# Kernel tuning notes

Measured on AMD Instinct MI355X. Metric: run time of the kernel, lower is better.

The kernel has to match this reference:

```python
import jax, jax.numpy as jnp
import numpy as np

K = 4            # kNN neighbors (edge_conv k=4)
HEADS = 4
HID = 32
NEG_SLOPE = 0.2  # PyG GATConv leaky_relu default


def knn_idx(x, k):
    # x: [N, C]. Pairwise squared distances via gram trick, self excluded.
    N = x.shape[0]
    sq = jnp.sum(x * x, axis=1)
    d = sq[:, None] + sq[None, :] - 2.0 * (x @ x.T)          # [N, N]
    r = jnp.arange(N)
    d = d.at[r, r].set(jnp.inf)                               # no self in kNN
    _, idx = jax.lax.top_k(-d, k)                             # [N, k] nearest
    return idx


def gat_layer(x, neigh, W, a_src, a_dst, b):
    # x: [N, C]; neigh: [N, k+1] (incl. self loop). PyG GATConv, concat=True.
    N = x.shape[0]
    h = (x @ W).reshape(N, HEADS, HID)                        # [N, H, D]
    asrc = jnp.einsum('nhd,hd->nh', h, a_src)                 # [N, H]
    adst = jnp.einsum('nhd,hd->nh', h, a_dst)                 # [N, H]
    e = jax.nn.leaky_relu(adst[:, None, :] + asrc[neigh], NEG_SLOPE)  # [N, k+1, H]
    attn = jax.nn.softmax(e, axis=1)                          # segment softmax (fixed fan-in)
    out = jnp.einsum('nkh,nkhd->nhd', attn, h[neigh])         # [N, H, D]
    return out.reshape(N, HEADS * HID) + b


def setup_inputs() -> dict:
    key = jax.random.key(0)
    ks = jax.random.split(key, 12)
    B, E, C = 256, 64, 32
    s = 0.1
    return {
        'x': jax.random.normal(ks[0], (B, E, C), jnp.float32),
        # DynamicEdgeConv MLP: Linear(2C->HID), ReLU, Linear(HID->HID)
        'mlp_w1': jax.random.normal(ks[1], (2 * C, HID), jnp.float32) * s,
        'mlp_b1': jnp.zeros((HID,), jnp.float32),
        'mlp_w2': jax.random.normal(ks[2], (HID, HID), jnp.float32) * s,
        'mlp_b2': jnp.zeros((HID,), jnp.float32),
        # GATConv(HID, HID, heads=HEADS, concat=True)
        'gat_w': jax.random.normal(ks[3], (C, HEADS * HID), jnp.float32) * s,
        'gat_asrc': jax.random.normal(ks[4], (HEADS, HID), jnp.float32) * s,
        'gat_adst': jax.random.normal(ks[5], (HEADS, HID), jnp.float32) * s,
        'gat_b': jnp.zeros((HEADS * HID,), jnp.float32),
        # fc: Linear(HID*HEADS -> num_classes)
        'fc_w': jax.random.normal(ks[6], (HEADS * HID, 2), jnp.float32) * s,
        'fc_b': jnp.zeros((2,), jnp.float32),
    }


def reference(x, mlp_w1, mlp_b1, mlp_w2, mlp_b2, gat_w, gat_asrc, gat_adst, gat_b, fc_w, fc_b):
    B, E, C = x.shape
    N = B * E
    xf = x.reshape(N, C)
    idx = knn_idx(xf, K)                                      # [N, K] int32
    # EdgeConv message MLP + max pool (edge_attr is discarded by the original forward)
    xi = xf[:, None, :]                                       # [N, 1, C]
    xj = xf[idx]                                              # [N, K, C]
    ef = jnp.concatenate([jnp.broadcast_to(xi, xj.shape), xj - xi], axis=-1)
    ef = jax.nn.relu(ef @ mlp_w1 + mlp_b1) @ mlp_w2 + mlp_b2
    _edge_attr = ef.max(axis=1)                               # [N, HID], unused downstream
    # GAT with self loops (PyG add_self_loops=True)
    neigh = jnp.concatenate([idx, jnp.arange(N)[:, None]], axis=1)  # [N, K+1]
    h = gat_layer(xf, neigh, gat_w, gat_asrc, gat_adst, gat_b)
    h = jax.nn.elu(h)
    h = h.reshape(B, E, HEADS * HID).mean(axis=1)             # [B, H*D]
    return h @ fc_w + fc_b                                    # [B, num_classes]
```

## Files before the change

kernel.cpp:

```cpp
#include <hip/hip_runtime.h>
#include <math.h>

#define N_PTS   16384
#define NT      1024
#define NCHUNK  32
#define JT_CH   (NT/NCHUNK)
#define SUBT    16
#define NSUB    (JT_CH/SUBT)
#define NS      16
#define JSPLIT  4
#define NPB     256

typedef __attribute__((ext_vector_type(4))) float f32x4;
typedef __attribute__((ext_vector_type(8))) _Float16 half8;

union H8 { half8 h; float4 f; };

#define MED3(a,b,c) __builtin_amdgcn_fmed3f((a),(b),(c))

#define INS4(c, A0, A1, A2, A3) {        \
  float n0_ = fmaxf(A0, c);              \
  float n1_ = MED3(A0, A1, c);           \
  float n2_ = MED3(A1, A2, c);           \
  float n3_ = MED3(A2, A3, c);           \
  A0 = n0_; A1 = n1_; A2 = n2_; A3 = n3_; }

__device__ __forceinline__ unsigned long long pack_key(float a, int j) {
  unsigned u = __float_as_uint(a);
  unsigned ord = u ^ (unsigned)(((int)u >> 31) | 0x80000000);
  unsigned m = ~ord;
  return ((unsigned long long)m << 32) | (unsigned)j;
}

__global__ __launch_bounds__(64) void k_prep(
    const float* __restrict__ x, float4* __restrict__ fragHi,
    float4* __restrict__ fragLo, float* __restrict__ nsq,
    unsigned* __restrict__ gcnt, unsigned long long* __restrict__ gbuf,
    unsigned* __restrict__ bcnt, float2* __restrict__ pmax)
{
  int p = blockIdx.x * 64 + threadIdx.x;
  const float4* xp = (const float4*)(x + (size_t)p * 32);
  int tile = p >> 4, lb = p & 15;
  float sq = 0.f, hn2 = 0.f, ln2 = 0.f;
  #pragma unroll
  for (int g = 0; g < 4; ++g) {
    float4 va = xp[g * 2], vb = xp[g * 2 + 1];
    float f[8] = {va.x, va.y, va.z, va.w, vb.x, vb.y, vb.z, vb.w};
    H8 hh, hl;
    #pragma unroll
    for (int e = 0; e < 8; ++e) {
      sq = fmaf(f[e], f[e], sq);
      _Float16 hi = (_Float16)f[e];
      _Float16 lo = (_Float16)(f[e] - (float)hi);
      hh.h[e] = hi; hl.h[e] = lo;
      float hf = (float)hi, lf = (float)lo;
      hn2 = fmaf(hf, hf, hn2);
      ln2 = fmaf(lf, lf, ln2);
    }
    int a = tile * 64 + g * 16 + lb;
    fragHi[a] = hh.f; fragLo[a] = hl.f;
  }
  nsq[p] = -0.5f * sq;
  gcnt[p] = 0u;
  #pragma unroll
  for (int e = 0; e < NS; ++e) gbuf[(size_t)p * NS + e] = ~0ull;
  if (blockIdx.x == 0 && threadIdx.x < NCHUNK) bcnt[threadIdx.x] = 0u;

  #pragma unroll
  for (int off = 32; off; off >>= 1) {
    hn2 = fmaxf(hn2, __shfl_xor(hn2, off));
    ln2 = fmaxf(ln2, __shfl_xor(ln2, off));
  }
  if (threadIdx.x == 0) pmax[blockIdx.x] = make_float2(hn2, ln2);
}

__global__ __launch_bounds__(256, 4) void k_knnA(
    const float4* __restrict__ fragHi, const float* __restrict__ nsq,
    float* __restrict__ cvals,
    const float* __restrict__ x, const float* __restrict__ gw,
    const float* __restrict__ aw_s, const float* __restrict__ aw_d,
    float* __restrict__ h, float* __restrict__ asrc, float* __restrict__ adst)
{
  __shared__ half8 sHi[SUBT * 64];
  __shared__ float sNq[SUBT * 16];

  const int tid = threadIdx.x;
  const int cy = blockIdx.y;

  if (cy >= NCHUNK) {
    const int fb = (cy - NCHUNK) * 64 + blockIdx.x;
    const int d = tid & 127, half = tid >> 7;
    const int head = d >> 5, hid = d & 31;

    float gwr[32];
    #pragma unroll
    for (int k = 0; k < 32; ++k) gwr[k] = gw[k * 128 + d];
    const float ws_ = aw_s[head * 32 + hid], wd_ = aw_d[head * 32 + hid];

    #pragma unroll
    for (int p = 0; p < 8; ++p) {
      int nl = (p << 1) | half;
      int n = fb * 16 + nl;
      const float4* xr = (const float4*)(x + (size_t)n * 32);
      float acc = 0.f;
      #pragma unroll
      for (int r = 0; r < 8; ++r) {
        float4 v = xr[r];
        acc = fmaf(v.x, gwr[r * 4 + 0], acc);
        acc = fmaf(v.y, gwr[r * 4 + 1], acc);
        acc = fmaf(v.z, gwr[r * 4 + 2], acc);
        acc = fmaf(v.w, gwr[r * 4 + 3], acc);
      }
      h[(size_t)n * 128 + d] = acc;
      float ps = acc * ws_, pd = acc * wd_;
      #pragma unroll
      for (int off = 16; off; off >>= 1) {
        ps += __shfl_xor(ps, off, 32);
        pd += __shfl_xor(pd, off, 32);
      }
      if (hid == 0) { asrc[n * 4 + head] = ps; adst[n * 4 + head] = pd; }
    }
    return;
  }

  const int w = tid >> 6, lane = tid & 63;
  const int grp = lane >> 4, col = lane & 15;
  const int itbase = blockIdx.x * 16 + w * 4;
  const bool blkdiag = ((int)(blockIdx.x >> 1) == cy);

  const half8* fH8 = (const half8*)fragHi;

  half8 bh[4];
  #pragma unroll
  for (int s = 0; s < 4; ++s)
    bh[s] = fH8[(size_t)(itbase + s) * 64 + lane];
  const bool dg0 = (col == grp * 4 + 0), dg1 = (col == grp * 4 + 1);
  const bool dg2 = (col == grp * 4 + 2), dg3 = (col == grp * 4 + 3);

  float La1[4];
  #pragma unroll
  for (int s = 0; s < 4; ++s) La1[s] = -3.4e38f;

  for (int sc = 0; sc < NSUB; ++sc) {
    int jt0 = cy * JT_CH + sc * SUBT;
    __syncthreads();
    const float4* gH = fragHi + (size_t)jt0 * 64;
    float4* dH = (float4*)sHi;
    #pragma unroll
    for (int r = 0; r < 4; ++r)
      dH[tid + r * 256] = gH[tid + r * 256];
    sNq[tid] = nsq[jt0 * 16 + tid];
    __syncthreads();

    for (int t = 0; t < SUBT; ++t) {
      half8 ah = sHi[t * 64 + lane];
      f32x4 q = *(const f32x4*)&sNq[t * 16 + grp * 4];
      int jt = jt0 + t;
      #pragma unroll
      for (int s = 0; s < 4; ++s) {
        f32x4 acc = __builtin_amdgcn_mfma_f32_16x16x32_f16(ah, bh[s], q, 0, 0, 0);
        if (blkdiag && jt == itbase + s) {
          acc.x = dg0 ? -3.4e38f : acc.x;
          acc.y = dg1 ? -3.4e38f : acc.y;
          acc.z = dg2 ? -3.4e38f : acc.z;
          acc.w = dg3 ? -3.4e38f : acc.w;
        }
        float t3 = fmaxf(fmaxf(acc.x, acc.y), acc.z);
        La1[s] = fmaxf(fmaxf(t3, acc.w), La1[s]);
      }
    }
  }

  #pragma unroll
  for (int s = 0; s < 4; ++s) {
    float m = La1[s];
    m = fmaxf(m, __shfl_xor(m, 16));
    m = fmaxf(m, __shfl_xor(m, 32));
    if (grp == 0) {
      int row = (itbase + s) * 16 + col;
      cvals[(size_t)cy * N_PTS + row] = m;
    }
  }
}

__global__ __launch_bounds__(128) void k_tauwl(
    const float* __restrict__ cvals, float* __restrict__ tau,
    unsigned* __restrict__ bcnt, int* __restrict__ bucket,
    const float2* __restrict__ pmax)
{
  __shared__ unsigned lcnt[NCHUNK];
  __shared__ unsigned gbase[NCHUNK];
  __shared__ int stage[NCHUNK][64];
  __shared__ float4 sL[64];
  __shared__ float sT[64];
  __shared__ float sEps;

  const int tid = threadIdx.x;
  const int lrow = tid & 63, half = tid >> 6;
  const int row = blockIdx.x * 64 + lrow;
  if (tid < NCHUNK) lcnt[tid] = 0u;

  if (tid < 64) {
    float hm = 0.f, lm = 0.f;
    #pragma unroll
    for (int k = 0; k < NPB / 64; ++k) {
      float2 v = pmax[tid + k * 64];
      hm = fmaxf(hm, v.x);
      lm = fmaxf(lm, v.y);
    }
    #pragma unroll
    for (int off = 32; off; off >>= 1) {
      hm = fmaxf(hm, __shfl_xor(hm, off));
      lm = fmaxf(lm, __shfl_xor(lm, off));
    }
    if (tid == 0) sEps = 4.4f * sqrtf(hm) * sqrtf(lm) + 1e-3f;
  }
  __syncthreads();
  const float eps = sEps;

  float A0 = -3.4e38f, A1 = -3.4e38f, A2 = -3.4e38f, A3 = -3.4e38f;
  float cm[16];
  #pragma unroll
  for (int k = 0; k < 16; ++k) {
    cm[k] = cvals[(size_t)(half * 16 + k) * N_PTS + row];
    INS4(cm[k], A0, A1, A2, A3);
  }
  if (half == 1) sL[lrow] = make_float4(A0, A1, A2, A3);
  __syncthreads();
  if (half == 0) {
    float4 o = sL[lrow];
    INS4(o.x, A0, A1, A2, A3);
    INS4(o.y, A0, A1, A2, A3);
    INS4(o.z, A0, A1, A2, A3);
    INS4(o.w, A0, A1, A2, A3);
    float theta = A3 - eps;
    sT[lrow] = theta;
    tau[row] = theta;
  }
  __syncthreads();
  const float tt = sT[lrow];
  #pragma unroll
  for (int k = 0; k < 16; ++k) {
    if (cm[k] >= tt) {
      int c = half * 16 + k;
      unsigned p = atomicAdd(&lcnt[c], 1u);
      stage[c][p] = row;
    }
  }
  __syncthreads();
  if (tid < NCHUNK) gbase[tid] = atomicAdd(bcnt + tid, lcnt[tid]);
  __syncthreads();
  for (int c = 0; c < NCHUNK; ++c) {
    unsigned n = lcnt[c], gb = gbase[c];
    for (unsigned k = tid; k < n; k += 128)
      bucket[c * N_PTS + gb + k] = stage[c][k];
  }
}

__global__ __launch_bounds__(256) void k_knnBW(
    const float4* __restrict__ fragHi, const float4* __restrict__ fragLo,
    const float* __restrict__ nsq, const float* __restrict__ tau,
    const unsigned* __restrict__ bcnt, const int* __restrict__ bucket,
    unsigned* __restrict__ gcnt, unsigned long long* __restrict__ gbuf)
{
  const int c = blockIdx.x;
  const int jseg = blockIdx.y >> 8;
  const unsigned n = bcnt[c];
  const unsigned base = (unsigned)(blockIdx.y & 255) * 64;
  if (base >= n) return;

  __shared__ int   sRow[64];
  __shared__ float sTau[64];

  const int tid = threadIdx.x;
  const int w = tid >> 6, lane = tid & 63;
  const int grp = lane >> 4, col = lane & 15;
  const float INF = __int_as_float(0x7f800000);

  if (tid < 64) {
    unsigned idx = base + tid;
    int myrow = (idx < n) ? bucket[c * N_PTS + idx] : -1;
    sRow[tid] = myrow;
    sTau[tid] = (myrow >= 0) ? tau[myrow] : INF;
  }
  __syncthreads();

  const half8* fH8 = (const half8*)fragHi;
  const half8* fL8 = (const half8*)fragLo;

  half8 bh[4], bl[4];
  int   rS[4];
  float tS[4];
  #pragma unroll
  for (int s = 0; s < 4; ++s) {
    int r = sRow[s * 16 + col];
    rS[s] = r;
    tS[s] = sTau[s * 16 + col];
    int rr = r < 0 ? 0 : r;
    size_t a = (size_t)(rr >> 4) * 64 + grp * 16 + (rr & 15);
    bh[s] = fH8[a];
    bl[s] = fL8[a];
  }

  const int jt0 = c * JT_CH + jseg * (JT_CH / JSPLIT) + w * (JT_CH / (JSPLIT * 4));
  #pragma unroll
  for (int ti = 0; ti < JT_CH / (JSPLIT * 4); ++ti) {
    int jt = jt0 + ti;
    half8 ah = fH8[(size_t)jt * 64 + lane];
    half8 al = fL8[(size_t)jt * 64 + lane];
    f32x4 q = *(const f32x4*)&nsq[jt * 16 + grp * 4];
    #pragma unroll
    for (int s = 0; s < 4; ++s) {
      f32x4 acc = __builtin_amdgcn_mfma_f32_16x16x32_f16(ah, bh[s], q, 0, 0, 0);
      acc = __builtin_amdgcn_mfma_f32_16x16x32_f16(ah, bl[s], acc, 0, 0, 0);
      acc = __builtin_amdgcn_mfma_f32_16x16x32_f16(al, bh[s], acc, 0, 0, 0);
      int jbase = jt * 16 + grp * 4;
      acc.x = (jbase + 0 == rS[s]) ? -3.4e38f : acc.x;
      acc.y = (jbase + 1 == rS[s]) ? -3.4e38f : acc.y;
      acc.z = (jbase + 2 == rS[s]) ? -3.4e38f : acc.z;
      acc.w = (jbase + 3 == rS[s]) ? -3.4e38f : acc.w;
      float m = fmaxf(fmaxf(acc.x, acc.y), fmaxf(acc.z, acc.w));
      if (__ballot(m >= tS[s])) {
        float av[4] = {acc.x, acc.y, acc.z, acc.w};
        #pragma unroll
        for (int e = 0; e < 4; ++e) {
          if (av[e] >= tS[s]) {
            unsigned sl = atomicAdd(gcnt + rS[s], 1u);
            if (sl < (unsigned)NS) gbuf[(size_t)rS[s] * NS + sl] = pack_key(av[e], jbase + e);
          }
        }
      }
    }
  }
}

__global__ __launch_bounds__(256) void k_gat(
    const float* __restrict__ h, const float* __restrict__ asrc, const float* __restrict__ adst,
    const unsigned long long* __restrict__ gbuf, const float* __restrict__ gb,
    float* __restrict__ mo_part)
{
  int b2 = blockIdx.x;
  int b = b2 >> 2, qq = b2 & 3;
  int tid = threadIdx.x;
  __shared__ int4 sknn[16];
  if (tid < 16) {
    int row = b * 64 + qq * 16 + tid;
    unsigned long long K0 = ~0ull, K1 = ~0ull, K2 = ~0ull, K3 = ~0ull;
    const unsigned long long* src = gbuf + (size_t)row * NS;
    #pragma unroll
    for (int e = 0; e < NS; ++e) {
      unsigned long long cc = src[e];
      bool g = cc < K3, c0 = cc < K0, c1 = cc < K1, c2 = cc < K2;
      unsigned long long n1 = c0 ? K0 : (c1 ? cc : K1);
      unsigned long long n2 = c1 ? K1 : (c2 ? cc : K2);
      unsigned long long n3 = c2 ? K2 : (g ? cc : K3);
      K0 = c0 ? cc : K0; K1 = n1; K2 = n2; K3 = n3;
    }
    sknn[tid] = make_int4((int)(unsigned)K0, (int)(unsigned)K1,
                          (int)(unsigned)K2, (int)(unsigned)K3);
  }
  __syncthreads();

  int w = tid >> 6, lane = tid & 63;
  int da = lane, db = lane + 64;
  int ha = lane >> 5, hb = ha + 2;
  float acca = 0.f, accb = 0.f;

  #pragma unroll
  for (int t = 0; t < 4; ++t) {
    int nl = t * 4 + w;
    int n = b * 64 + qq * 16 + nl;
    int4 nb = sknn[nl];
    int nbs[5] = {nb.x, nb.y, nb.z, nb.w, n};
    float ad_a = adst[n * 4 + ha], ad_b = adst[n * 4 + hb];
    float ea[5], eb[5];
    #pragma unroll
    for (int k = 0; k < 5; ++k) {
      float va = ad_a + asrc[nbs[k] * 4 + ha];
      float vb = ad_b + asrc[nbs[k] * 4 + hb];
      ea[k] = va > 0.f ? va : 0.2f * va;
      eb[k] = vb > 0.f ? vb : 0.2f * vb;
    }
    float ma = ea[0], mb = eb[0];
    #pragma unroll
    for (int k = 1; k < 5; ++k) { ma = fmaxf(ma, ea[k]); mb = fmaxf(mb, eb[k]); }
    float sa = 0.f, sb = 0.f;
    #pragma unroll
    for (int k = 0; k < 5; ++k) {
      ea[k] = __expf(ea[k] - ma); sa += ea[k];
      eb[k] = __expf(eb[k] - mb); sb += eb[k];
    }
    float outa = 0.f, outb = 0.f;
    #pragma unroll
    for (int k = 0; k < 5; ++k) {
      const float* hr = h + (size_t)nbs[k] * 128;
      outa = fmaf(ea[k], hr[da], outa);
      outb = fmaf(eb[k], hr[db], outb);
    }
    outa = outa / sa + gb[da];
    outb = outb / sb + gb[db];
    acca += outa > 0.f ? outa : expm1f(outa);
    accb += outb > 0.f ? outb : expm1f(outb);
  }

  __shared__ float red[4][128];
  red[w][da] = acca; red[w][db] = accb;
  __syncthreads();
  if (tid < 128) {
    float s = (red[0][tid] + red[1][tid] + red[2][tid] + red[3][tid]) * (1.f / 64.f);
    mo_part[b2 * 128 + tid] = s;
  }
}

__global__ __launch_bounds__(64) void k_fc(
    const float* __restrict__ mo_part, const float* __restrict__ fw, const float* __restrict__ fb,
    float* __restrict__ out)
{
  int b = blockIdx.x, lane = threadIdx.x;
  float m0 = 0.f, m1 = 0.f;
  #pragma unroll
  for (int q = 0; q < 4; ++q) {
    m0 += mo_part[(b * 4 + q) * 128 + lane];
    m1 += mo_part[(b * 4 + q) * 128 + lane + 64];
  }
  float p0 = m0 * fw[lane * 2]     + m1 * fw[(lane + 64) * 2];
  float p1 = m0 * fw[lane * 2 + 1] + m1 * fw[(lane + 64) * 2 + 1];
  #pragma unroll
  for (int off = 32; off; off >>= 1) {
    p0 += __shfl_xor(p0, off, 64);
    p1 += __shfl_xor(p1, off, 64);
  }
  if (lane == 0) { out[b * 2] = p0 + fb[0]; out[b * 2 + 1] = p1 + fb[1]; }
}

extern "C" void kernel_launch(void* const* d_in, const int* in_sizes, int n_in,
                              void* d_out, int out_size, void* d_ws, size_t ws_size,
                              hipStream_t stream)
{
  const float* x   = (const float*)d_in[0];
  const float* gw  = (const float*)d_in[5];
  const float* as_ = (const float*)d_in[6];
  const float* ad_ = (const float*)d_in[7];
  const float* gb  = (const float*)d_in[8];
  const float* fw  = (const float*)d_in[9];
  const float* fb  = (const float*)d_in[10];

  char* ws = (char*)d_ws;
  float*  cvals  = (float*)(ws);
  float*  h      = (float*)(ws + 2097152);
  float*  asrc   = (float*)(ws + 10485760);
  float*  adst   = (float*)(ws + 10747904);
  float4* fragHi = (float4*)(ws + 11010048);
  float4* fragLo = (float4*)(ws + 12058624);
  float*  nsq    = (float*)(ws + 13107200);
  float*  tau    = (float*)(ws + 13172736);
  unsigned* gcnt = (unsigned*)(ws + 13238272);
  unsigned long long* gbuf = (unsigned long long*)(ws + 13303808);
  unsigned* bcnt = (unsigned*)(ws + 15400960);
  float2* pmax   = (float2*)(ws + 15401216);
  int*    bucket = (int*)   (ws + 15403264);
  float*  mo_part= (float*)(ws + 17500416);
  float*  outp   = (float*)d_out;

  k_prep<<<NPB, 64, 0, stream>>>(x, fragHi, fragLo, nsq, gcnt, gbuf, bcnt, pmax);
  k_knnA<<<dim3(64, NCHUNK + 16), 256, 0, stream>>>(fragHi, nsq, cvals,
                                                    x, gw, as_, ad_, h, asrc, adst);
  k_tauwl<<<N_PTS / 64, 128, 0, stream>>>(cvals, tau, bcnt, bucket, pmax);
  k_knnBW<<<dim3(NCHUNK, 256 * JSPLIT), 256, 0, stream>>>(fragHi, fragLo, nsq, tau,
                                                          bcnt, bucket, gcnt, gbuf);
  k_gat<<<1024, 256, 0, stream>>>(h, asrc, adst, gbuf, gb, mo_part);
  k_fc<<<256, 64, 0, stream>>>(mo_part, fw, fb, outp);
}
```

Baseline: 94.26 us.

## Refine kNN candidate pruning to sub-chunk granularity of 16 tiles

The coarse pass now records a per-row max for each 16-tile sub-chunk (64 sub-chunks instead of 32 chunks). The threshold kernel buckets rows per sub-chunk, and the exact pass launches one block column per sub-chunk over only 16 tiles. Rows are re-checked only against sub-chunks that can contain a near neighbour, which cuts exact-pass work. In exchange it doubles cvals storage and reads, adds work and register pressure to the threshold kernel, and moves the workspace layout around.

Measured after the change: 197.5 us. +109.5%, slower.

```diff
diff --git a/kernel.cpp b/kernel.cpp
--- a/kernel.cpp
+++ b/kernel.cpp
@@ -7,8 +7,9 @@
 #define JT_CH   (NT/NCHUNK)
 #define SUBT    16
 #define NSUB    (JT_CH/SUBT)
+#define NSC     (NCHUNK*NSUB)
+#define JT_SC   16
 #define NS      16
-#define JSPLIT  4
 #define NPB     256
 
 typedef __attribute__((ext_vector_type(4))) float f32x4;
@@ -64,7 +65,7 @@
   gcnt[p] = 0u;
   #pragma unroll
   for (int e = 0; e < NS; ++e) gbuf[(size_t)p * NS + e] = ~0ull;
-  if (blockIdx.x == 0 && threadIdx.x < NCHUNK) bcnt[threadIdx.x] = 0u;
+  if (blockIdx.x == 0 && threadIdx.x < NSC) bcnt[threadIdx.x] = 0u;
 
   #pragma unroll
   for (int off = 32; off; off >>= 1) {
@@ -137,10 +138,6 @@
   const bool dg0 = (col == grp * 4 + 0), dg1 = (col == grp * 4 + 1);
   const bool dg2 = (col == grp * 4 + 2), dg3 = (col == grp * 4 + 3);
 
-  float La1[4];
-  #pragma unroll
-  for (int s = 0; s < 4; ++s) La1[s] = -3.4e38f;
-
   for (int sc = 0; sc < NSUB; ++sc) {
     int jt0 = cy * JT_CH + sc * SUBT;
     __syncthreads();
@@ -151,6 +148,10 @@
       dH[tid + r * 256] = gH[tid + r * 256];
     sNq[tid] = nsq[jt0 * 16 + tid];
     __syncthreads();
+
+    float La1[4];
+    #pragma unroll
+    for (int s = 0; s < 4; ++s) La1[s] = -3.4e38f;
 
     for (int t = 0; t < SUBT; ++t) {
       half8 ah = sHi[t * 64 + lane];
@@ -169,16 +170,16 @@
         La1[s] = fmaxf(fmaxf(t3, acc.w), La1[s]);
       }
     }
-  }
-
-  #pragma unroll
-  for (int s = 0; s < 4; ++s) {
-    float m = La1[s];
-    m = fmaxf(m, __shfl_xor(m, 16));
-    m = fmaxf(m, __shfl_xor(m, 32));
-    if (grp == 0) {
-      int row = (itbase + s) * 16 + col;
-      cvals[(size_t)cy * N_PTS + row] = m;
+
+    #pragma unroll
+    for (int s = 0; s < 4; ++s) {
+      float m = La1[s];
+      m = fmaxf(m, __shfl_xor(m, 16));
+      m = fmaxf(m, __shfl_xor(m, 32));
+      if (grp == 0) {
+        int row = (itbase + s) * 16 + col;
+        cvals[(size_t)(cy * NSUB + sc) * N_PTS + row] = m;
+      }
     }
   }
 }
@@ -188,9 +189,9 @@
     unsigned* __restrict__ bcnt, int* __restrict__ bucket,
     const float2* __restrict__ pmax)
 {
-  __shared__ unsigned lcnt[NCHUNK];
-  __shared__ unsigned gbase[NCHUNK];
-  __shared__ int stage[NCHUNK][64];
+  __shared__ unsigned lcnt[NSC];
+  __shared__ unsigned gbase[NSC];
+  __shared__ int stage[NSC][64];
   __shared__ float4 sL[64];
   __shared__ float sT[64];
   __shared__ float sEps;
@@ -198,7 +199,7 @@
   const int tid = threadIdx.x;
   const int lrow = tid & 63, half = tid >> 6;
   const int row = blockIdx.x * 64 + lrow;
-  if (tid < NCHUNK) lcnt[tid] = 0u;
+  if (tid < NSC) lcnt[tid] = 0u;
 
   if (tid < 64) {
     float hm = 0.f, lm = 0.f;
@@ -219,10 +220,10 @@
   const float eps = sEps;
 
   float A0 = -3.4e38f, A1 = -3.4e38f, A2 = -3.4e38f, A3 = -3.4e38f;
-  float cm[16];
-  #pragma unroll
-  for (int k = 0; k < 16; ++k) {
-    cm[k] = cvals[(size_t)(half * 16 + k) * N_PTS + row];
+  float cm[32];
+  #pragma unroll
+  for (int k = 0; k < 32; ++k) {
+    cm[k] = cvals[(size_t)(half * 32 + k) * N_PTS + row];
     INS4(cm[k], A0, A1, A2, A3);
   }
   if (half == 1) sL[lrow] = make_float4(A0, A1, A2, A3);
@@ -240,17 +241,17 @@
   __syncthreads();
   const float tt = sT[lrow];
   #pragma unroll
-  for (int k = 0; k < 16; ++k) {
+  for (int k = 0; k < 32; ++k) {
     if (cm[k] >= tt) {
-      int c = half * 16 + k;
+      int c = half * 32 + k;
       unsigned p = atomicAdd(&lcnt[c], 1u);
       stage[c][p] = row;
     }
   }
   __syncthreads();
-  if (tid < NCHUNK) gbase[tid] = atomicAdd(bcnt + tid, lcnt[tid]);
-  __syncthreads();
-  for (int c = 0; c < NCHUNK; ++c) {
+  if (tid < NSC) gbase[tid] = atomicAdd(bcnt + tid, lcnt[tid]);
+  __syncthreads();
+  for (int c = 0; c < NSC; ++c) {
     unsigned n = lcnt[c], gb = gbase[c];
     for (unsigned k = tid; k < n; k += 128)
       bucket[c * N_PTS + gb + k] = stage[c][k];
@@ -264,9 +265,8 @@
     unsigned* __restrict__ gcnt, unsigned long long* __restrict__ gbuf)
 {
   const int c = blockIdx.x;
-  const int jseg = blockIdx.y >> 8;
   const unsigned n = bcnt[c];
-  const unsigned base = (unsigned)(blockIdx.y & 255) * 64;
+  const unsigned base = blockIdx.y * 64;
   if (base >= n) return;
 
   __shared__ int   sRow[64];
@@ -302,9 +302,9 @@
     bl[s] = fL8[a];
   }
 
-  const int jt0 = c * JT_CH + jseg * (JT_CH / JSPLIT) + w * (JT_CH / (JSPLIT * 4));
-  #pragma unroll
-  for (int ti = 0; ti < JT_CH / (JSPLIT * 4); ++ti) {
+  const int jt0 = c * JT_SC + w * (JT_SC / 4);
+  #pragma unroll
+  for (int ti = 0; ti < JT_SC / 4; ++ti) {
     int jt = jt0 + ti;
     half8 ah = fH8[(size_t)jt * 64 + lane];
     half8 al = fL8[(size_t)jt * 64 + lane];
@@ -447,27 +447,27 @@
 
   char* ws = (char*)d_ws;
   float*  cvals  = (float*)(ws);
-  float*  h      = (float*)(ws + 2097152);
-  float*  asrc   = (float*)(ws + 10485760);
-  float*  adst   = (float*)(ws + 10747904);
-  float4* fragHi = (float4*)(ws + 11010048);
-  float4* fragLo = (float4*)(ws + 12058624);
-  float*  nsq    = (float*)(ws + 13107200);
-  float*  tau    = (float*)(ws + 13172736);
-  unsigned* gcnt = (unsigned*)(ws + 13238272);
-  unsigned long long* gbuf = (unsigned long long*)(ws + 13303808);
-  unsigned* bcnt = (unsigned*)(ws + 15400960);
-  float2* pmax   = (float2*)(ws + 15401216);
-  int*    bucket = (int*)   (ws + 15403264);
-  float*  mo_part= (float*)(ws + 17500416);
+  float*  mo_part= (float*)(ws);
+  float*  h      = (float*)(ws + 4194304);
+  float*  asrc   = (float*)(ws + 12582912);
+  float*  adst   = (float*)(ws + 12845056);
+  float4* fragHi = (float4*)(ws + 13107200);
+  float4* fragLo = (float4*)(ws + 14155776);
+  float*  nsq    = (float*)(ws + 15204352);
+  float*  tau    = (float*)(ws + 15269888);
+  unsigned* gcnt = (unsigned*)(ws + 15335424);
+  unsigned long long* gbuf = (unsigned long long*)(ws + 15400960);
+  unsigned* bcnt = (unsigned*)(ws + 17498112);
+  float2* pmax   = (float2*)(ws + 17498624);
+  int*    bucket = (int*)   (ws + 17500672);
   float*  outp   = (float*)d_out;
 
   k_prep<<<NPB, 64, 0, stream>>>(x, fragHi, fragLo, nsq, gcnt, gbuf, bcnt, pmax);
   k_knnA<<<dim3(64, NCHUNK + 16), 256, 0, stream>>>(fragHi, nsq, cvals,
                                                     x, gw, as_, ad_, h, asrc, adst);
   k_tauwl<<<N_PTS / 64, 128, 0, stream>>>(cvals, tau, bcnt, bucket, pmax);
-  k_knnBW<<<dim3(NCHUNK, 256 * JSPLIT), 256, 0, stream>>>(fragHi, fragLo, nsq, tau,
-                                                          bcnt, bucket, gcnt, gbuf);
+  k_knnBW<<<dim3(NSC, 256), 256, 0, stream>>>(fragHi, fragLo, nsq, tau,
+                                              bcnt, bucket, gcnt, gbuf);
   k_gat<<<1024, 256, 0, stream>>>(h, asrc, adst, gbuf, gb, mo_part);
   k_fc<<<256, 64, 0, stream>>>(mo_part, fw, fb, outp);
 }
```
